# Kernel optimization log

Measured on AMD Instinct MI355X. Metric: run time of the kernel, lower is better.

Reference implementation:

```python
import jax, jax.numpy as jnp
import numpy as np

B, S, D = 2, 2048, 2048
H, HD = 16, 128


def _rope_cos_sin(seq_len, head_dim, base=10000.0):
    inv_freq = 1.0 / (base ** (np.arange(0, head_dim, 2, dtype=np.float32) / head_dim))
    t = np.arange(seq_len, dtype=np.float32)
    freqs = np.outer(t, inv_freq)                      # [S, HD/2]
    emb = np.concatenate([freqs, freqs], axis=-1)      # [S, HD]
    return jnp.asarray(np.cos(emb)), jnp.asarray(np.sin(emb))


def setup_inputs() -> dict:
    key = jax.random.key(0)
    k1, k2, k3 = jax.random.split(key, 3)
    hidden_states = jax.random.normal(k1, (B, S, D), dtype=jnp.float32)
    cos, sin = _rope_cos_sin(S, HD)
    # qkv weight: [3, H*HD, D] as in CastedLinear(batch_output_dims=(3,))
    w_qkv = jax.random.normal(k2, (3, H * HD, D), dtype=jnp.float32) * (1.0 / D ** 0.5)
    w_o = jax.random.normal(k3, (D, H * HD), dtype=jnp.float32) * (1.0 / (H * HD) ** 0.5)
    return {"hidden_states": hidden_states, "cos": cos, "sin": sin, "w_qkv": w_qkv, "w_o": w_o}


def _rotate_half(x):
    x1, x2 = jnp.split(x, 2, axis=-1)
    return jnp.concatenate([-x2, x1], axis=-1)


def _apply_rope(x, cos, sin):
    # x: [B, S, H, HD]; cos/sin: [S, HD] -> broadcast over heads via [:, None, :]
    return x * cos[:, None, :] + _rotate_half(x) * sin[:, None, :]


def reference(hidden_states, cos, sin, w_qkv, w_o):
    # fused QKV projection: weight flattened to [3*H*HD, D]
    qkv = jnp.einsum('bsd,fd->bsf', hidden_states, w_qkv.reshape(-1, D))  # [B,S,3*H*HD]
    # rearrange '... (h hd) -> ... h hd' with h=H  ->  [B,S,H,3*HD], then chunk
    qkv = qkv.reshape(B, S, H, 3 * HD)
    q, k, v = jnp.split(qkv, 3, axis=-1)          # each [B,S,H,HD]
    q = _apply_rope(q, cos, sin)
    k = _apply_rope(k, cos, sin)
    # SDPA, causal
    scale = 1.0 / jnp.sqrt(jnp.asarray(HD, dtype=q.dtype))
    scores = jnp.einsum('bshd,bthd->bhst', q, k) * scale      # [B,H,S,S]
    causal = jnp.tril(jnp.ones((S, S), dtype=bool))
    scores = jnp.where(causal, scores, jnp.asarray(-jnp.inf, dtype=scores.dtype))
    probs = jax.nn.softmax(scores, axis=-1)
    attn = jnp.einsum('bhst,bthd->bshd', probs, v)            # [B,S,H,HD]
    attn = attn.reshape(B, S, H * HD)
    return jnp.einsum('bsf,df->bsd', attn, w_o)               # [B,S,D]
```

## Files before the change

### kernel.cpp

```cpp
#include <hip/hip_runtime.h>

typedef unsigned short u16;
typedef __bf16 bf16x8 __attribute__((ext_vector_type(8)));
typedef float f32x4 __attribute__((ext_vector_type(4)));


__device__ __forceinline__ u16 f2bf(float x) {
  __bf16 h = (__bf16)x;
  return __builtin_bit_cast(u16, h);
}

__device__ __forceinline__ void async_copy16(void* lds, const void* g) {
  __builtin_amdgcn_global_load_lds((const __attribute__((address_space(1))) void*)g,
                                   (__attribute__((address_space(3))) void*)lds, 16, 0, 0);
}

__global__ __launch_bounds__(256) void cast_all(const float* __restrict__ hidden,
                                                const float* __restrict__ wqkv,
                                                const float* __restrict__ wo,
                                                u16* __restrict__ xb,
                                                u16* __restrict__ wqb,
                                                u16* __restrict__ wob) {
  int i = blockIdx.x * 256 + threadIdx.x;
  const float* s;
  u16* d;
  int off;
  if (i < 2097152) { s = hidden; d = xb; off = i; }
  else if (i < 2097152 + 3145728) { s = wqkv; d = wqb; off = i - 2097152; }
  else { s = wo; d = wob; off = i - (2097152 + 3145728); }
  float4 v = ((const float4*)s)[off];
  ushort4 o;
  o.x = f2bf(v.x); o.y = f2bf(v.y); o.z = f2bf(v.z); o.w = f2bf(v.w);
  ((ushort4*)d)[off] = o;
}

__global__ __launch_bounds__(256) void gemm_qkv(const u16* __restrict__ A,
                                                const u16* __restrict__ W,
                                                const float* __restrict__ cosb,
                                                const float* __restrict__ sinb,
                                                u16* __restrict__ Qb,
                                                u16* __restrict__ Kb,
                                                u16* __restrict__ Vt) {
  __shared__ __align__(16) u16 As[128 * 64];
  __shared__ __align__(16) u16 Bs[128 * 64];
  const int tid = threadIdx.x;
  const int lane = tid & 63;
  const int wave = tid >> 6;
  const int wm = (wave >> 1) * 64;
  const int r16 = lane & 15;
  const int g4 = lane >> 4;
  const int rsw = r16 & 7;
  const int bm = blockIdx.x * 128;
  const int bn = blockIdx.y * 128;

  size_t aoff[4], boff[4];
  u16* ldsA[4];
  u16* ldsB[4];
#pragma unroll
  for (int i = 0; i < 4; i++) {
    int row = wave * 32 + i * 8 + (lane >> 3);
    int c = (lane & 7) ^ (row & 7);
    aoff[i] = (size_t)(bm + row) * 2048 + c * 8;
    boff[i] = (size_t)(bn + row) * 2048 + c * 8;
    ldsA[i] = &As[(wave * 4 + i) * 512];
    ldsB[i] = &Bs[(wave * 4 + i) * 512];
  }

  int bcol[4];
#pragma unroll
  for (int n = 0; n < 4; n++) bcol[n] = (wave & 1) * 32 + (n & 1) * 16 + (n >> 1) * 64;

  f32x4 acc[4][4];
  f32x4 zero = {0.0f, 0.0f, 0.0f, 0.0f};
#pragma unroll
  for (int m = 0; m < 4; m++)
#pragma unroll
    for (int n = 0; n < 4; n++) acc[m][n] = zero;

  for (int kt = 0; kt < 2048; kt += 64) {
    __syncthreads();
#pragma unroll
    for (int i = 0; i < 4; i++) {
      async_copy16(ldsA[i], A + aoff[i] + kt);
      async_copy16(ldsB[i], W + boff[i] + kt);
    }
    __syncthreads();
#pragma unroll
    for (int ks = 0; ks < 2; ks++) {
      bf16x8 af[4], bfr[4];
#pragma unroll
      for (int m = 0; m < 4; m++)
        af[m] = *(const bf16x8*)(&As[(wm + m * 16 + r16) * 64 + ((ks * 4 + g4) ^ rsw) * 8]);
#pragma unroll
      for (int n = 0; n < 4; n++)
        bfr[n] = *(const bf16x8*)(&Bs[(bcol[n] + r16) * 64 + ((ks * 4 + g4) ^ rsw) * 8]);
#pragma unroll
      for (int m = 0; m < 4; m++)
#pragma unroll
        for (int n = 0; n < 4; n++)
          acc[m][n] = __builtin_amdgcn_mfma_f32_16x16x32_bf16(af[m], bfr[n], acc[m][n], 0, 0, 0);
    }
  }

  const int which = blockIdx.y % 3;
  const int hh = blockIdx.y / 3;
  const float qs = (which == 0) ? 0.08838834764831845f * 1.4426950408889634f : 1.0f;
#pragma unroll
  for (int m = 0; m < 4; m++) {
#pragma unroll
    for (int r = 0; r < 4; r++) {
      int row = bm + wm + m * 16 + g4 * 4 + r;
      int bb = row >> 11;
      int s = row & 2047;
      size_t bhIdx = (size_t)(bb * 16 + hh);
      if (which == 2) {
#pragma unroll
        for (int n = 0; n < 4; n++) {
          int hd = bcol[n] + r16;
          Vt[(bhIdx * 128 + hd) * 2048 + s] = f2bf(acc[m][n][r]);
        }
      } else {
        u16* dst = (which ? Kb : Qb) + (bhIdx * 2048 + s) * 128;
#pragma unroll
        for (int n = 0; n < 2; n++) {
          int hd = bcol[n] + r16;
          float c = cosb[s * 128 + hd] * qs;
          float sn = sinb[s * 128 + hd] * qs;
          float x1 = acc[m][n][r], x2 = acc[m][n + 2][r];
          dst[hd] = f2bf(x1 * c - x2 * sn);
          dst[hd + 64] = f2bf(x2 * c + x1 * sn);
        }
      }
    }
  }
}

__global__ __launch_bounds__(512) void flash_attn(const u16* __restrict__ Q,
                                                  const u16* __restrict__ K,
                                                  const u16* __restrict__ Vt,
                                                  u16* __restrict__ O) {
  __shared__ __align__(16) u16 Ks[2][128 * 128];
  __shared__ __align__(16) u16 Vs[2][128 * 128];
  __shared__ __align__(16) u16 Ps[8 * 16 * 64];
  const int tid = threadIdx.x;
  const int lane = tid & 63;
  const int wave = tid >> 6;
  const int bh = blockIdx.y;
  const int r16 = lane & 15;
  const int g4 = lane >> 4;
  const int rsw = r16 & 7;
  const u16* Qh = Q + (size_t)bh * 2048 * 128;
  const u16* Kh = K + (size_t)bh * 2048 * 128;
  const u16* Vh = Vt + (size_t)bh * 128 * 2048;
  const int b = bh >> 4;
  const int h = bh & 15;

  int koff[4], voff[4], ldsOff[4];
#pragma unroll
  for (int i = 0; i < 4; i++) {
    int r = (wave * 4 + i) * 4 + (lane >> 4);
    int c = (lane & 15) ^ (r & 7);
    koff[i] = r * 128 + c * 8;
    voff[i] = r * 2048 + c * 8;
    ldsOff[i] = (wave * 4 + i) * 512;
  }

#pragma unroll 1
  for (int pass = 0; pass < 2; pass++) {
    const int T = pass == 0 ? (int)blockIdx.x : 15 - (int)blockIdx.x;
    const int qg = T * 128 + wave * 16 + r16;
    const int nk = T + 1;

    bf16x8 qf[4];
#pragma unroll
    for (int ks = 0; ks < 4; ks++)
      qf[ks] = *(const bf16x8*)(Qh + (size_t)qg * 128 + ks * 32 + g4 * 8);

    f32x4 o[8];
    f32x4 zero = {0.0f, 0.0f, 0.0f, 0.0f};
#pragma unroll
    for (int c = 0; c < 8; c++) o[c] = zero;
    float m_i = -__builtin_inff();
    float l_i = 0.0f;

    __syncthreads();
#pragma unroll
    for (int i = 0; i < 4; i++) {
      async_copy16(&Ks[0][ldsOff[i]], Kh + koff[i]);
      async_copy16(&Vs[0][ldsOff[i]], Vh + voff[i]);
    }

    int cur = 0;
    for (int u = 0; u < nk; u++) {
      __syncthreads();
      if (u + 1 < nk) {
#pragma unroll
        for (int i = 0; i < 4; i++) {
          async_copy16(&Ks[cur ^ 1][ldsOff[i]], Kh + (size_t)(u + 1) * 16384 + koff[i]);
          async_copy16(&Vs[cur ^ 1][ldsOff[i]], Vh + (size_t)(u + 1) * 128 + voff[i]);
        }
      }

      f32x4 sacc[8];
#pragma unroll
      for (int n = 0; n < 8; n++) sacc[n] = zero;
#pragma unroll
      for (int n = 0; n < 8; n++) {
#pragma unroll
        for (int ks = 0; ks < 4; ks++) {
          bf16x8 kf = *(const bf16x8*)(&Ks[cur][(n * 16 + r16) * 128 + ((ks * 4 + g4) ^ rsw) * 8]);
          sacc[n] = __builtin_amdgcn_mfma_f32_16x16x32_bf16(kf, qf[ks], sacc[n], 0, 0, 0);
        }
      }

      if (u == nk - 1) {
#pragma unroll
        for (int n = 0; n < 8; n++)
#pragma unroll
          for (int r = 0; r < 4; r++) {
            int key = u * 128 + 16 * n + g4 * 4 + r;
            if (key > qg) sacc[n][r] = -__builtin_inff();
          }
      }
      float vmax = -__builtin_inff();
#pragma unroll
      for (int n = 0; n < 8; n++)
#pragma unroll
        for (int r = 0; r < 4; r++) vmax = fmaxf(vmax, sacc[n][r]);
      vmax = fmaxf(vmax, __shfl_xor(vmax, 16));
      vmax = fmaxf(vmax, __shfl_xor(vmax, 32));
      float mn = fmaxf(m_i, vmax);
      float alpha = exp2f(m_i - mn);
      m_i = mn;

#pragma unroll
      for (int c = 0; c < 8; c++)
#pragma unroll
        for (int r = 0; r < 4; r++) o[c][r] *= alpha;

      float ssum = 0.0f;
      u16* Pw = &Ps[wave * 1024];
#pragma unroll
      for (int half = 0; half < 2; half++) {
#pragma unroll
        for (int nl = 0; nl < 4; nl++) {
          int n = half * 4 + nl;
          float p0 = exp2f(sacc[n][0] - mn);
          float p1 = exp2f(sacc[n][1] - mn);
          float p2 = exp2f(sacc[n][2] - mn);
          float p3 = exp2f(sacc[n][3] - mn);
          ssum += (p0 + p1) + (p2 + p3);
          ushort4 pk;
          pk.x = f2bf(p0); pk.y = f2bf(p1); pk.z = f2bf(p2); pk.w = f2bf(p3);
          *(ushort4*)(&Pw[r16 * 64 + ((2 * nl + (g4 >> 1)) ^ rsw) * 8 + (g4 & 1) * 4]) = pk;
        }
#pragma unroll
        for (int ks2 = 0; ks2 < 2; ks2++) {
          bf16x8 pf = *(const bf16x8*)(&Pw[r16 * 64 + ((ks2 * 4 + g4) ^ rsw) * 8]);
          int kv = half * 2 + ks2;
#pragma unroll
          for (int c = 0; c < 8; c++) {
            bf16x8 vf = *(const bf16x8*)(&Vs[cur][(c * 16 + r16) * 128 + ((kv * 4 + g4) ^ rsw) * 8]);
            o[c] = __builtin_amdgcn_mfma_f32_16x16x32_bf16(vf, pf, o[c], 0, 0, 0);
          }
        }
      }
      ssum += __shfl_xor(ssum, 16);
      ssum += __shfl_xor(ssum, 32);
      l_i = l_i * alpha + ssum;
      cur ^= 1;
    }

    float rl = 1.0f / l_i;
    u16* dst = O + ((size_t)(b * 2048 + qg)) * 2048 + h * 128;
#pragma unroll
    for (int c = 0; c < 8; c++) {
      ushort4 pk;
      pk.x = f2bf(o[c][0] * rl);
      pk.y = f2bf(o[c][1] * rl);
      pk.z = f2bf(o[c][2] * rl);
      pk.w = f2bf(o[c][3] * rl);
      *(ushort4*)(dst + c * 16 + g4 * 4) = pk;
    }
  }
}

__global__ __launch_bounds__(256) void gemm_out(const u16* __restrict__ A,
                                                const u16* __restrict__ W,
                                                float* __restrict__ out) {
  __shared__ __align__(16) u16 As[128 * 64];
  __shared__ __align__(16) u16 Bs[128 * 64];
  const int tid = threadIdx.x;
  const int lane = tid & 63;
  const int wave = tid >> 6;
  const int wm = (wave >> 1) * 64;
  const int wn = (wave & 1) * 64;
  const int r16 = lane & 15;
  const int g4 = lane >> 4;
  const int rsw = r16 & 7;
  const int bm = blockIdx.x * 128;
  const int bn = blockIdx.y * 128;

  size_t aoff[4], boff[4];
  u16* ldsA[4];
  u16* ldsB[4];
#pragma unroll
  for (int i = 0; i < 4; i++) {
    int row = wave * 32 + i * 8 + (lane >> 3);
    int c = (lane & 7) ^ (row & 7);
    aoff[i] = (size_t)(bm + row) * 2048 + c * 8;
    boff[i] = (size_t)(bn + row) * 2048 + c * 8;
    ldsA[i] = &As[(wave * 4 + i) * 512];
    ldsB[i] = &Bs[(wave * 4 + i) * 512];
  }

  f32x4 acc[4][4];
  f32x4 zero = {0.0f, 0.0f, 0.0f, 0.0f};
#pragma unroll
  for (int m = 0; m < 4; m++)
#pragma unroll
    for (int n = 0; n < 4; n++) acc[m][n] = zero;

  for (int kt = 0; kt < 2048; kt += 64) {
    __syncthreads();
#pragma unroll
    for (int i = 0; i < 4; i++) {
      async_copy16(ldsA[i], A + aoff[i] + kt);
      async_copy16(ldsB[i], W + boff[i] + kt);
    }
    __syncthreads();
#pragma unroll
    for (int ks = 0; ks < 2; ks++) {
      bf16x8 af[4], bfr[4];
#pragma unroll
      for (int m = 0; m < 4; m++)
        af[m] = *(const bf16x8*)(&As[(wm + m * 16 + r16) * 64 + ((ks * 4 + g4) ^ rsw) * 8]);
#pragma unroll
      for (int n = 0; n < 4; n++)
        bfr[n] = *(const bf16x8*)(&Bs[(wn + n * 16 + r16) * 64 + ((ks * 4 + g4) ^ rsw) * 8]);
#pragma unroll
      for (int m = 0; m < 4; m++)
#pragma unroll
        for (int n = 0; n < 4; n++)
          acc[m][n] = __builtin_amdgcn_mfma_f32_16x16x32_bf16(af[m], bfr[n], acc[m][n], 0, 0, 0);
    }
  }

#pragma unroll
  for (int m = 0; m < 4; m++) {
#pragma unroll
    for (int n = 0; n < 4; n++) {
#pragma unroll
      for (int r = 0; r < 4; r++) {
        int row = bm + wm + m * 16 + g4 * 4 + r;
        int col = bn + wn + n * 16 + r16;
        out[(size_t)row * 2048 + col] = acc[m][n][r];
      }
    }
  }
}

extern "C" void kernel_launch(void* const* d_in, const int* in_sizes, int n_in,
                              void* d_out, int out_size, void* d_ws, size_t ws_size,
                              hipStream_t stream) {
  const float* hidden = (const float*)d_in[0];
  const float* cosb   = (const float*)d_in[1];
  const float* sinb   = (const float*)d_in[2];
  const float* w_qkv  = (const float*)d_in[3];
  const float* w_o    = (const float*)d_in[4];
  float* out = (float*)d_out;

  char* ws = (char*)d_ws;
  u16* Xbf    = (u16*)(ws);
  u16* Wqkvbf = (u16*)(ws + 16777216);
  u16* Wobf   = (u16*)(ws + 41943040);
  u16* Qb     = (u16*)(ws + 50331648);
  u16* Kb     = (u16*)(ws + 67108864);
  u16* Vt     = (u16*)(ws + 83886080);
  u16* Ob     = (u16*)(ws + 100663296);

  cast_all<<<24576, 256, 0, stream>>>(hidden, w_qkv, w_o, Xbf, Wqkvbf, Wobf);
  gemm_qkv<<<dim3(32, 48), 256, 0, stream>>>(Xbf, Wqkvbf, cosb, sinb, Qb, Kb, Vt);
  flash_attn<<<dim3(8, 32), 512, 0, stream>>>(Qb, Kb, Vt, Ob);
  gemm_out<<<dim3(32, 16), 256, 0, stream>>>(Ob, Wobf, out);
}
```

Before: 402.7 us.

## Rewrite QKV GEMM as 256x256 double-buffered, phase-scheduled MFMA pipeline

```diff
diff --git a/kernel.cpp b/kernel.cpp
--- a/kernel.cpp
+++ b/kernel.cpp
@@ -1,6 +1,7 @@
 #include <hip/hip_runtime.h>
 
 typedef unsigned short u16;
+typedef unsigned int u32;
 typedef __bf16 bf16x8 __attribute__((ext_vector_type(8)));
 typedef float f32x4 __attribute__((ext_vector_type(4)));
 
@@ -34,99 +35,194 @@
   ((ushort4*)d)[off] = o;
 }
 
-__global__ __launch_bounds__(256) void gemm_qkv(const u16* __restrict__ A,
-                                                const u16* __restrict__ W,
-                                                const float* __restrict__ cosb,
-                                                const float* __restrict__ sinb,
-                                                u16* __restrict__ Qb,
-                                                u16* __restrict__ Kb,
-                                                u16* __restrict__ Vt) {
-  __shared__ __align__(16) u16 As[128 * 64];
-  __shared__ __align__(16) u16 Bs[128 * 64];
+
+__device__ __forceinline__ void lda4(bf16x8 (&af)[4][2], const u16* base, int row, int c0, int c1) {
+#pragma unroll
+  for (int mf = 0; mf < 4; mf++) {
+    const u16* p = base + (row + mf * 16) * 64;
+    af[mf][0] = *(const bf16x8*)(p + c0);
+    af[mf][1] = *(const bf16x8*)(p + c1);
+  }
+}
+
+__device__ __forceinline__ void ldb2(bf16x8 (&bfr)[2][2], const u16* base, int row, int c0, int c1) {
+#pragma unroll
+  for (int nf = 0; nf < 2; nf++) {
+    const u16* p = base + (row + nf * 16) * 64;
+    bfr[nf][0] = *(const bf16x8*)(p + c0);
+    bfr[nf][1] = *(const bf16x8*)(p + c1);
+  }
+}
+
+#define FENCE() asm volatile("" ::: "memory")
+#define LGKM0() asm volatile("s_waitcnt lgkmcnt(0)" ::: "memory")
+#define VMW4() asm volatile("s_waitcnt vmcnt(4)" ::: "memory")
+#define VMW0() asm volatile("s_waitcnt vmcnt(0)" ::: "memory")
+#define BAR() __builtin_amdgcn_s_barrier()
+#define PH_TOP() \
+  FENCE(); BAR(); LGKM0(); __builtin_amdgcn_sched_barrier(0); __builtin_amdgcn_s_setprio(1)
+#define PH_BOT() __builtin_amdgcn_s_setprio(0); FENCE(); BAR()
+
+#define MFMA_Q(MH, NH)                                                                   \
+  _Pragma("unroll") for (int ks = 0; ks < 2; ks++)                                       \
+  _Pragma("unroll") for (int mf = 0; mf < 4; mf++)                                       \
+  _Pragma("unroll") for (int nf = 0; nf < 2; nf++)                                       \
+      acc[(MH)*4 + mf][(NH)*2 + nf] = __builtin_amdgcn_mfma_f32_16x16x32_bf16(           \
+          af[mf][ks], bfr[nf][ks], acc[(MH)*4 + mf][(NH)*2 + nf], 0, 0, 0);
+
+#define STG_A(DB, H, KT)                                                                   \
+  {                                                                                        \
+    async_copy16(ldsA + (DB)*32768 + ((H)*64 + w8) * 128, Ag + aoff[H][0] + (KT)*128);     \
+    async_copy16(ldsA + (DB)*32768 + (128 + (H)*64 + w8) * 128, Ag + aoff[H][1] + (KT)*128); \
+  }
+#define STG_B(DB, H, KT)                                                                   \
+  {                                                                                        \
+    async_copy16(ldsB + (DB)*32768 + ((H)*64 + w8) * 128, Bg + boff[H][0] + (KT)*128);     \
+    async_copy16(ldsB + (DB)*32768 + (128 + (H)*64 + w8) * 128, Bg + boff[H][1] + (KT)*128); \
+  }
+
+template <bool MORE>
+__device__ __forceinline__ void qkv_iter(const u16* As, const u16* Bs, char* ldsA, char* ldsB,
+                                         const char* Ag, const char* Bg,
+                                         const u32 (&aoff)[2][2], const u32 (&boff)[2][2],
+                                         int w8, int arow0, int brow0, int c0, int c1,
+                                         int k1, int k2, int k3,
+                                         bf16x8 (&af)[4][2], bf16x8 (&bfr)[2][2],
+                                         f32x4 (&acc)[8][4]) {
+  const int arow1 = arow0 + 256;
+  const int brow1 = brow0 + 256;
+  lda4(af, As, arow0, c0, c1);
+  ldb2(bfr, Bs, brow0, c0, c1);
+  STG_A(1, 1, k1);
+  PH_TOP(); MFMA_Q(0, 0); PH_BOT();
+  ldb2(bfr, Bs, brow0 + 64, c0, c1);
+  STG_B(1, 0, k1);
+  PH_TOP(); MFMA_Q(0, 1); PH_BOT();
+  lda4(af, As, arow0 + 64, c0, c1);
+  if (MORE) { STG_A(0, 0, k2); }
+  PH_TOP(); MFMA_Q(1, 1); PH_BOT();
+  ldb2(bfr, Bs, brow0, c0, c1);
+  if (MORE) { STG_B(0, 1, k2); }
+  PH_TOP(); MFMA_Q(1, 0);
+  __builtin_amdgcn_s_setprio(0);
+  if (MORE) { VMW4(); } else { VMW0(); }
+  FENCE(); BAR();
+  lda4(af, As, arow1, c0, c1);
+  ldb2(bfr, Bs, brow1, c0, c1);
+  if (MORE) { STG_A(0, 1, k2); }
+  PH_TOP(); MFMA_Q(0, 0); PH_BOT();
+  ldb2(bfr, Bs, brow1 + 64, c0, c1);
+  if (MORE) { STG_B(0, 0, k2); }
+  PH_TOP(); MFMA_Q(0, 1); PH_BOT();
+  lda4(af, As, arow1 + 64, c0, c1);
+  if (MORE) { STG_A(1, 0, k3); }
+  PH_TOP(); MFMA_Q(1, 1); PH_BOT();
+  ldb2(bfr, Bs, brow1, c0, c1);
+  if (MORE) { STG_B(1, 1, k3); }
+  PH_TOP(); MFMA_Q(1, 0);
+  __builtin_amdgcn_s_setprio(0);
+  if (MORE) { VMW4(); } else { VMW0(); }
+  FENCE(); BAR();
+}
+
+__global__ __launch_bounds__(512, 2) void gemm_qkv(const u16* __restrict__ A,
+                                                   const u16* __restrict__ W,
+                                                   const float* __restrict__ cosb,
+                                                   const float* __restrict__ sinb,
+                                                   u16* __restrict__ Qb,
+                                                   u16* __restrict__ Kb,
+                                                   u16* __restrict__ Vt) {
+  extern __shared__ u16 smem[];
+  u16* As = smem;
+  u16* Bs = smem + 32768;
+  char* ldsA = (char*)As;
+  char* ldsB = (char*)Bs;
+  const char* Ag = (const char*)A;
+  const char* Bg = (const char*)W;
+
   const int tid = threadIdx.x;
   const int lane = tid & 63;
-  const int wave = tid >> 6;
-  const int wm = (wave >> 1) * 64;
+  const int w = tid >> 6;
+  const int wm = w >> 2;
+  const int wn = w & 3;
   const int r16 = lane & 15;
   const int g4 = lane >> 4;
   const int rsw = r16 & 7;
-  const int bm = blockIdx.x * 128;
-  const int bn = blockIdx.y * 128;
-
-  size_t aoff[4], boff[4];
-  u16* ldsA[4];
-  u16* ldsB[4];
-#pragma unroll
-  for (int i = 0; i < 4; i++) {
-    int row = wave * 32 + i * 8 + (lane >> 3);
-    int c = (lane & 7) ^ (row & 7);
-    aoff[i] = (size_t)(bm + row) * 2048 + c * 8;
-    boff[i] = (size_t)(bn + row) * 2048 + c * 8;
-    ldsA[i] = &As[(wave * 4 + i) * 512];
-    ldsB[i] = &Bs[(wave * 4 + i) * 512];
-  }
-
-  int bcol[4];
-#pragma unroll
-  for (int n = 0; n < 4; n++) bcol[n] = (wave & 1) * 32 + (n & 1) * 16 + (n >> 1) * 64;
-
-  f32x4 acc[4][4];
-  f32x4 zero = {0.0f, 0.0f, 0.0f, 0.0f};
-#pragma unroll
-  for (int m = 0; m < 4; m++)
-#pragma unroll
-    for (int n = 0; n < 4; n++) acc[m][n] = zero;
-
-  for (int kt = 0; kt < 2048; kt += 64) {
-    __syncthreads();
-#pragma unroll
-    for (int i = 0; i < 4; i++) {
-      async_copy16(ldsA[i], A + aoff[i] + kt);
-      async_copy16(ldsB[i], W + boff[i] + kt);
-    }
-    __syncthreads();
-#pragma unroll
-    for (int ks = 0; ks < 2; ks++) {
-      bf16x8 af[4], bfr[4];
-#pragma unroll
-      for (int m = 0; m < 4; m++)
-        af[m] = *(const bf16x8*)(&As[(wm + m * 16 + r16) * 64 + ((ks * 4 + g4) ^ rsw) * 8]);
-#pragma unroll
-      for (int n = 0; n < 4; n++)
-        bfr[n] = *(const bf16x8*)(&Bs[(bcol[n] + r16) * 64 + ((ks * 4 + g4) ^ rsw) * 8]);
-#pragma unroll
-      for (int m = 0; m < 4; m++)
-#pragma unroll
-        for (int n = 0; n < 4; n++)
-          acc[m][n] = __builtin_amdgcn_mfma_f32_16x16x32_bf16(af[m], bfr[n], acc[m][n], 0, 0, 0);
-    }
-  }
-
-  const int which = blockIdx.y % 3;
-  const int hh = blockIdx.y / 3;
+  const int w8 = w * 8;
+  const int l8 = lane >> 3;
+  const int gch = (lane & 7) ^ l8;
+
+  const int nblk = blockIdx.x;
+  const int swz = (nblk & 7) * 48 + (nblk >> 3);
+  const int bm = (swz & 15) * 256;
+  const int by = swz >> 4;
+  const int bn = by * 256;
+
+  u32 aoff[2][2], boff[2][2];
+#pragma unroll
+  for (int h = 0; h < 2; h++) {
+#pragma unroll
+    for (int j = 0; j < 2; j++) {
+      int row = j * 128 + h * 64 + w8 + l8;
+      aoff[h][j] = (u32)(bm + row) * 4096u + (u32)gch * 16u;
+      boff[h][j] = (u32)(bn + row) * 4096u + (u32)gch * 16u;
+    }
+  }
+
+  const int c0 = (g4 ^ rsw) * 8;
+  const int c1 = ((4 + g4) ^ rsw) * 8;
+  const int arow0 = wm * 128 + r16;
+  const int brow0 = (wn >> 1) * 128 + (wn & 1) * 32 + r16;
+
+  bf16x8 af[4][2], bfr[2][2];
+  f32x4 acc[8][4];
+  const f32x4 fzero = {0.0f, 0.0f, 0.0f, 0.0f};
+#pragma unroll
+  for (int i = 0; i < 8; i++)
+#pragma unroll
+    for (int j = 0; j < 4; j++) acc[i][j] = fzero;
+
+  STG_A(0, 0, 0); STG_B(0, 0, 0); STG_A(0, 1, 0); STG_B(0, 1, 0);
+  STG_A(1, 0, 1); STG_B(1, 1, 1);
+  VMW4();
+  FENCE(); BAR();
+
+#pragma unroll 1
+  for (int t = 0; t < 15; t++) {
+    qkv_iter<true>(As, Bs, ldsA, ldsB, Ag, Bg, aoff, boff, w8, arow0, brow0, c0, c1,
+                   2 * t + 1, 2 * t + 2, 2 * t + 3, af, bfr, acc);
+  }
+  qkv_iter<false>(As, Bs, ldsA, ldsB, Ag, Bg, aoff, boff, w8, arow0, brow0, c0, c1,
+                  31, 31, 31, af, bfr, acc);
+
+  const int blk128 = by * 2 + (wn >> 1);
+  const int which = blk128 % 3;
+  const int head = blk128 / 3;
   const float qs = (which == 0) ? 0.08838834764831845f * 1.4426950408889634f : 1.0f;
-#pragma unroll
-  for (int m = 0; m < 4; m++) {
+  const int hb = (wn & 1) * 32;
+
+#pragma unroll
+  for (int mi = 0; mi < 8; mi++) {
 #pragma unroll
     for (int r = 0; r < 4; r++) {
-      int row = bm + wm + m * 16 + g4 * 4 + r;
+      int row = bm + wm * 128 + mi * 16 + g4 * 4 + r;
       int bb = row >> 11;
       int s = row & 2047;
-      size_t bhIdx = (size_t)(bb * 16 + hh);
+      size_t bhIdx = (size_t)(bb * 16 + head);
       if (which == 2) {
 #pragma unroll
-        for (int n = 0; n < 4; n++) {
-          int hd = bcol[n] + r16;
-          Vt[(bhIdx * 128 + hd) * 2048 + s] = f2bf(acc[m][n][r]);
+        for (int ni = 0; ni < 4; ni++) {
+          int hd = hb + (ni & 1) * 16 + (ni >> 1) * 64 + r16;
+          Vt[(bhIdx * 128 + hd) * 2048 + s] = f2bf(acc[mi][ni][r]);
         }
       } else {
-        u16* dst = (which ? Kb : Qb) + (bhIdx * 2048 + s) * 128;
-#pragma unroll
-        for (int n = 0; n < 2; n++) {
-          int hd = bcol[n] + r16;
+        u16* dst = (which ? Kb : Qb) + (bhIdx * 2048 + (size_t)s) * 128;
+#pragma unroll
+        for (int ni = 0; ni < 2; ni++) {
+          int hd = hb + ni * 16 + r16;
           float c = cosb[s * 128 + hd] * qs;
           float sn = sinb[s * 128 + hd] * qs;
-          float x1 = acc[m][n][r], x2 = acc[m][n + 2][r];
+          float x1 = acc[mi][ni][r], x2 = acc[mi][ni + 2][r];
           dst[hd] = f2bf(x1 * c - x2 * sn);
           dst[hd + 64] = f2bf(x2 * c + x1 * sn);
         }
@@ -134,6 +230,12 @@
     }
   }
 }
+
+#undef STG_A
+#undef STG_B
+#undef MFMA_Q
+#undef PH_TOP
+#undef PH_BOT
 
 __global__ __launch_bounds__(512) void flash_attn(const u16* __restrict__ Q,
                                                   const u16* __restrict__ K,
@@ -379,8 +481,15 @@
   u16* Vt     = (u16*)(ws + 83886080);
   u16* Ob     = (u16*)(ws + 100663296);
 
+  static int attr_done = 0;
+  if (!attr_done) {
+    (void)hipFuncSetAttribute((const void*)gemm_qkv,
+                              hipFuncAttributeMaxDynamicSharedMemorySize, 131072);
+    attr_done = 1;
+  }
+
   cast_all<<<24576, 256, 0, stream>>>(hidden, w_qkv, w_o, Xbf, Wqkvbf, Wobf);
-  gemm_qkv<<<dim3(32, 48), 256, 0, stream>>>(Xbf, Wqkvbf, cosb, sinb, Qb, Kb, Vt);
+  gemm_qkv<<<384, 512, 131072, stream>>>(Xbf, Wqkvbf, cosb, sinb, Qb, Kb, Vt);
   flash_attn<<<dim3(8, 32), 512, 0, stream>>>(Qb, Kb, Vt, Ob);
   gemm_out<<<dim3(32, 16), 256, 0, stream>>>(Ob, Wobf, out);
 }
```

Result: faster. 390.4 us (-3.1%).
